# Kernel optimization log

Measured on AMD Instinct MI355X. Metric: run time of the kernel, lower is better.

## Reference

```python
import jax, jax.numpy as jnp
import numpy as np

B, S, E = 4, 2048, 1024
H = 16
D = E // H  # head_dim = 64


def setup_inputs() -> dict:
    key = jax.random.key(0)
    k1, k2, k3 = jax.random.split(key, 3)
    x = jax.random.normal(k1, (B, S, E), dtype=jnp.float32)
    w_qkv = jax.random.normal(k2, (E, 3 * E), dtype=jnp.float32) * (E ** -0.5)
    b_qkv = jnp.zeros((3 * E,), dtype=jnp.float32)
    w_proj = jax.random.normal(k3, (E, E), dtype=jnp.float32) * (E ** -0.5)
    b_proj = jnp.zeros((E,), dtype=jnp.float32)
    return {"x": x, "w_qkv": w_qkv, "b_qkv": b_qkv, "w_proj": w_proj, "b_proj": b_proj}


def reference(x, w_qkv, b_qkv, w_proj, b_proj):
    bsz, seq_len, emb = x.shape
    scale = D ** -0.5
    qkv = x @ w_qkv + b_qkv                      # [B,S,3E]
    q, k, v = jnp.split(qkv, 3, axis=2)
    # [B,S,E] -> [B,H,S,D]
    q = q.reshape(bsz, seq_len, H, D).transpose(0, 2, 1, 3)
    k = k.reshape(bsz, seq_len, H, D).transpose(0, 2, 1, 3)
    v = v.reshape(bsz, seq_len, H, D).transpose(0, 2, 1, 3)
    att = jnp.einsum('bhqd,bhkd->bhqk', q, k) * scale
    causal = jnp.tril(jnp.ones((seq_len, seq_len), dtype=bool))
    att = jnp.where(causal, att, -jnp.inf)
    att = jax.nn.softmax(att, axis=-1)
    y = jnp.einsum('bhqk,bhkd->bhqd', att, v)
    y = y.transpose(0, 2, 1, 3).reshape(bsz, seq_len, emb)
    return y @ w_proj + b_proj
```

## Files before the change

kernel.cpp:

```cpp
#include <hip/hip_runtime.h>
#include <hip/hip_bf16.h>
#include <stdint.h>

#define S_LEN 2048
#define EMB   1024
#define NH    16
#define HD    64

typedef unsigned short u16;
typedef __attribute__((ext_vector_type(4))) float f32x4;
typedef __attribute__((ext_vector_type(8))) short bf16x8;

typedef __attribute__((address_space(1))) const unsigned char gas_t;
typedef __attribute__((address_space(3))) unsigned char las_t;

static __device__ __forceinline__ void gld_lds16(const void* g, void* l) {
  __builtin_amdgcn_global_load_lds((gas_t*)g, (las_t*)l, 16, 0, 0);
}

static __device__ __forceinline__ u16 f2bf(float f) {
  unsigned int u = __builtin_bit_cast(unsigned int, f);
  u = u + 0x7fffu + ((u >> 16) & 1u);
  return (u16)(u >> 16);
}

static __device__ __forceinline__ float fexp2(float x) {
  float r;
  asm("v_exp_f32 %0, %1" : "=v"(r) : "v"(x));
  return r;
}

static __device__ __forceinline__ unsigned cvt_pk_bf16(float lo, float hi) {
  unsigned r;
  asm("v_cvt_pk_bf16_f32 %0, %1, %2" : "=v"(r) : "v"(lo), "v"(hi));
  return r;
}

static __device__ __forceinline__ float red4rows_max(float x) {
  unsigned u = __builtin_bit_cast(unsigned, x);
  auto r = __builtin_amdgcn_permlane32_swap(u, u, false, false);
  float y = fmaxf(__builtin_bit_cast(float, (unsigned)r[0]),
                  __builtin_bit_cast(float, (unsigned)r[1]));
  unsigned v = __builtin_bit_cast(unsigned, y);
  auto r2 = __builtin_amdgcn_permlane16_swap(v, v, false, false);
  return fmaxf(__builtin_bit_cast(float, (unsigned)r2[0]),
               __builtin_bit_cast(float, (unsigned)r2[1]));
}
static __device__ __forceinline__ float red4rows_sum(float x) {
  unsigned u = __builtin_bit_cast(unsigned, x);
  auto r = __builtin_amdgcn_permlane32_swap(u, u, false, false);
  float y = __builtin_bit_cast(float, (unsigned)r[0]) +
            __builtin_bit_cast(float, (unsigned)r[1]);
  unsigned v = __builtin_bit_cast(unsigned, y);
  auto r2 = __builtin_amdgcn_permlane16_swap(v, v, false, false);
  return __builtin_bit_cast(float, (unsigned)r2[0]) +
         __builtin_bit_cast(float, (unsigned)r2[1]);
}

__global__ __launch_bounds__(256) void k_cvt(const float* __restrict__ in,
                                             u16* __restrict__ out, int n4) {
  int i = blockIdx.x * blockDim.x + threadIdx.x;
  int stride = gridDim.x * blockDim.x;
  for (; i < n4; i += stride) {
    float4 f = ((const float4*)in)[i];
    ushort4 o;
    o.x = f2bf(f.x); o.y = f2bf(f.y); o.z = f2bf(f.z); o.w = f2bf(f.w);
    ((ushort4*)out)[i] = o;
  }
}

__global__ __launch_bounds__(256) void k_transpose_cvt(const float* __restrict__ W,
                                                       u16* __restrict__ WT,
                                                       int K, int N) {
  __shared__ u16 tile[64][68];
  const int c0 = blockIdx.x * 64, r0 = blockIdx.y * 64;
  const int t = threadIdx.x;
  const int tr = t >> 4, tc4 = (t & 15) * 4;
#pragma unroll
  for (int i = 0; i < 4; i++) {
    const int r = tr + 16 * i;
    float4 f = *(const float4*)&W[(size_t)(r0 + r) * N + c0 + tc4];
    ushort4 o;
    o.x = f2bf(f.x); o.y = f2bf(f.y); o.z = f2bf(f.z); o.w = f2bf(f.w);
    *(ushort4*)&tile[r][tc4] = o;
  }
  __syncthreads();
  const int oc = t >> 2, or0 = (t & 3) * 16;
  u16 vals[16];
#pragma unroll
  for (int j = 0; j < 16; j++) vals[j] = tile[or0 + j][oc];
  u16* dst = &WT[(size_t)(c0 + oc) * K + r0 + or0];
  *(uint4*)dst = *(const uint4*)&vals[0];
  *(uint4*)(dst + 8) = *(const uint4*)&vals[8];
}

template <int MODE>
__global__ __launch_bounds__(256) void k_gemm(const u16* __restrict__ A,
                                              const u16* __restrict__ BT,
                                              const float* __restrict__ bias,
                                              float* __restrict__ Cout,
                                              u16* __restrict__ q_ws,
                                              u16* __restrict__ k_ws,
                                              u16* __restrict__ v_t,
                                              int N, int K) {
  __shared__ u16 As[2][128 * 32];
  __shared__ u16 Bs[2][128 * 32];
  const int tid = threadIdx.x;
  const int w = tid >> 6, lane = tid & 63;
  const int wr = w >> 1, wc = w & 1;
  const int lrow = lane & 15, lk8 = (lane >> 4) * 8;
  const int brow = blockIdx.y * 128, bcol = blockIdx.x * 128;
  const int srow = lane >> 2;
  const int scol = (lane & 3) * 8;

  const f32x4 zero = {0.f, 0.f, 0.f, 0.f};
  f32x4 acc[4][4];
#pragma unroll
  for (int m = 0; m < 4; m++)
#pragma unroll
    for (int n = 0; n < 4; n++) acc[m][n] = zero;

  auto stage = [&](int kt, int buf) {
#pragma unroll
    for (int i = 0; i < 2; i++) {
      const int c = w * 2 + i;
      const int row = c * 16 + srow;
      gld_lds16(&A[(size_t)(brow + row) * K + kt + scol], (void*)(&As[buf][c * 512]));
      gld_lds16(&BT[(size_t)(bcol + row) * K + kt + scol], (void*)(&Bs[buf][c * 512]));
    }
  };

  const int NK = K >> 5;
  stage(0, 0);
  __syncthreads();
  for (int it = 0; it < NK; ++it) {
    const int cur = it & 1;
    if (it + 1 < NK) stage((it + 1) << 5, cur ^ 1);
    bf16x8 af[4], bfr[4];
#pragma unroll
    for (int mt = 0; mt < 4; mt++)
      af[mt] = *(const bf16x8*)&As[cur][(wr * 64 + mt * 16 + lrow) * 32 + lk8];
#pragma unroll
    for (int nt = 0; nt < 4; nt++)
      bfr[nt] = *(const bf16x8*)&Bs[cur][(wc * 64 + nt * 16 + lrow) * 32 + lk8];
    __builtin_amdgcn_s_setprio(1);
#pragma unroll
    for (int mt = 0; mt < 4; mt++)
#pragma unroll
      for (int nt = 0; nt < 4; nt++)
        acc[mt][nt] = __builtin_amdgcn_mfma_f32_16x16x32_bf16(af[mt], bfr[nt],
                                                              acc[mt][nt], 0, 0, 0);
    __builtin_amdgcn_s_setprio(0);
    __syncthreads();
  }

  if constexpr (MODE == 0) {
    const int which = bcol >> 10;
#pragma unroll
    for (int mt = 0; mt < 4; mt++)
#pragma unroll
      for (int nt = 0; nt < 4; nt++) {
        const int col = bcol + wc * 64 + nt * 16 + lrow;
        const int e = col & 1023;
        const int h = e >> 6, d = e & 63;
        const int row0 = brow + wr * 64 + mt * 16 + (lane >> 4) * 4;
        const int b = row0 >> 11, s0 = row0 & 2047;
        const size_t bh = (size_t)(b * NH + h);
        const float bv = bias[col];
        if (which == 2) {
          ushort4 pk;
          pk.x = f2bf(acc[mt][nt][0] + bv);
          pk.y = f2bf(acc[mt][nt][1] + bv);
          pk.z = f2bf(acc[mt][nt][2] + bv);
          pk.w = f2bf(acc[mt][nt][3] + bv);
          *(ushort4*)&v_t[(bh * HD + d) * S_LEN + s0] = pk;
        } else {
          u16* dst = which ? k_ws : q_ws;
#pragma unroll
          for (int r = 0; r < 4; r++)
            dst[(bh * S_LEN + s0 + r) * HD + d] = f2bf(acc[mt][nt][r] + bv);
        }
      }
  } else {
#pragma unroll
    for (int mt = 0; mt < 4; mt++)
#pragma unroll
      for (int nt = 0; nt < 4; nt++)
#pragma unroll
        for (int r = 0; r < 4; r++) {
          const int row = brow + wr * 64 + mt * 16 + (lane >> 4) * 4 + r;
          const int col = bcol + wc * 64 + nt * 16 + lrow;
          Cout[(size_t)row * N + col] = acc[mt][nt][r] + bias[col];
        }
  }
}

__global__ __launch_bounds__(256, 2) void k_attn(const u16* __restrict__ q_ws,
                                                 const u16* __restrict__ k_ws,
                                                 const u16* __restrict__ v_t,
                                                 u16* __restrict__ y) {
  __shared__ u16 Kl[2][64 * 64];
  __shared__ u16 Vl[2][64 * 64];
  const int tid = threadIdx.x;
  const int w = tid >> 6, lane = tid & 63;
  const int lrow = lane & 15, lk8 = (lane >> 4) * 8;
  const int g4 = (lane >> 4) * 4;
  const int pr = blockIdx.x;
  const int tileA = pr, tileB = 31 - pr;
  const int bh = blockIdx.y;
  const size_t base = (size_t)bh * S_LEN * HD;
  const float SC = 0.125f * 1.4426950408889634f;

  bf16x8 qfA[2], qfB[2];
#pragma unroll
  for (int ks = 0; ks < 2; ks++) {
    qfA[ks] = *(const bf16x8*)&q_ws[base + (size_t)(tileA * 64 + w * 16 + lrow) * HD + ks * 32 + lk8];
    qfB[ks] = *(const bf16x8*)&q_ws[base + (size_t)(tileB * 64 + w * 16 + lrow) * HD + ks * 32 + lk8];
  }

  const f32x4 zero = {0.f, 0.f, 0.f, 0.f};
  f32x4 oA[4], oB[4];
#pragma unroll
  for (int dt = 0; dt < 4; dt++) { oA[dt] = zero; oB[dt] = zero; }
  float mA = -1e30f, lA = 0.f, mB = -1e30f, lB = 0.f;

  auto stage = [&](int jb, int buf) {
#pragma unroll
    for (int i = 0; i < 2; i++) {
      const int c = w * 2 + i;
      const int row = c * 8 + (lane >> 3);
      const int blk = (lane & 7) ^ (row & 7);
      gld_lds16(&k_ws[base + (size_t)(jb * 64 + row) * HD + blk * 8],
                (void*)(&Kl[buf][c * 512]));
      gld_lds16(&v_t[base + (size_t)row * S_LEN + jb * 64 + blk * 8],
                (void*)(&Vl[buf][c * 512]));
    }
  };

  auto process = [&](const bf16x8 (&kf)[2][4], const bf16x8 (&vf)[2][4],
                     const bf16x8 (&qf)[2], f32x4 (&o)[4], float& m_run,
                     float& l_run, bool maskDiag) {
    f32x4 sa[4];
#pragma unroll
    for (int nt = 0; nt < 4; nt++) sa[nt] = zero;
    __builtin_amdgcn_s_setprio(1);
#pragma unroll
    for (int ks = 0; ks < 2; ks++)
#pragma unroll
      for (int nt = 0; nt < 4; nt++)
        sa[nt] = __builtin_amdgcn_mfma_f32_16x16x32_bf16(kf[ks][nt], qf[ks], sa[nt], 0, 0, 0);
    __builtin_amdgcn_s_setprio(0);

    float sv[4][4];
    if (maskDiag) {
#pragma unroll
      for (int nt = 0; nt < 4; nt++)
#pragma unroll
        for (int r = 0; r < 4; r++) {
          float x = sa[nt][r] * SC;
          if ((nt * 16 + g4 + r) > (w * 16 + lrow)) x = -3.0e38f;
          sv[nt][r] = x;
        }
    } else {
#pragma unroll
      for (int nt = 0; nt < 4; nt++)
#pragma unroll
        for (int r = 0; r < 4; r++) sv[nt][r] = sa[nt][r] * SC;
    }

    float mx = fmaxf(fmaxf(fmaxf(sv[0][0], sv[0][1]), fmaxf(sv[0][2], sv[0][3])),
                     fmaxf(fmaxf(sv[1][0], sv[1][1]), fmaxf(sv[1][2], sv[1][3])));
    mx = fmaxf(mx,
               fmaxf(fmaxf(fmaxf(sv[2][0], sv[2][1]), fmaxf(sv[2][2], sv[2][3])),
                     fmaxf(fmaxf(sv[3][0], sv[3][1]), fmaxf(sv[3][2], sv[3][3]))));
    mx = red4rows_max(mx);
    const bool nogrow = __all(mx <= m_run + 8.0f);
    float mn = m_run;
    if (!nogrow) {
      mn = fmaxf(m_run, mx);
      const float alpha = fexp2(m_run - mn);
      l_run *= alpha;
#pragma unroll
      for (int dt = 0; dt < 4; dt++) o[dt] *= alpha;
      m_run = mn;
    }
    float sum = 0.f;
#pragma unroll
    for (int nt = 0; nt < 4; nt++)
#pragma unroll
      for (int r = 0; r < 4; r++) {
        const float p = fexp2(sv[nt][r] - mn);
        sv[nt][r] = p;
        sum += p;
      }
    sum = red4rows_sum(sum);
    l_run += sum;

    unsigned pk[4][2];
#pragma unroll
    for (int nt = 0; nt < 4; nt++) {
      pk[nt][0] = cvt_pk_bf16(sv[nt][0], sv[nt][1]);
      pk[nt][1] = cvt_pk_bf16(sv[nt][2], sv[nt][3]);
    }
    union { unsigned u[4]; bf16x8 v; } c0, c1;
    {
      auto r0 = __builtin_amdgcn_permlane32_swap(pk[0][0], pk[1][0], false, false);
      auto s0 = __builtin_amdgcn_permlane16_swap(r0[0], r0[1], false, false);
      auto r1 = __builtin_amdgcn_permlane32_swap(pk[0][1], pk[1][1], false, false);
      auto s1 = __builtin_amdgcn_permlane16_swap(r1[0], r1[1], false, false);
      c0.u[0] = s0[0]; c0.u[1] = s1[0]; c0.u[2] = s0[1]; c0.u[3] = s1[1];
      auto r2 = __builtin_amdgcn_permlane32_swap(pk[2][0], pk[3][0], false, false);
      auto s2 = __builtin_amdgcn_permlane16_swap(r2[0], r2[1], false, false);
      auto r3 = __builtin_amdgcn_permlane32_swap(pk[2][1], pk[3][1], false, false);
      auto s3 = __builtin_amdgcn_permlane16_swap(r3[0], r3[1], false, false);
      c1.u[0] = s2[0]; c1.u[1] = s3[0]; c1.u[2] = s2[1]; c1.u[3] = s3[1];
    }
    bf16x8 pfrag[2] = {c0.v, c1.v};

    __builtin_amdgcn_s_setprio(1);
#pragma unroll
    for (int ks = 0; ks < 2; ks++)
#pragma unroll
      for (int dt = 0; dt < 4; dt++)
        o[dt] = __builtin_amdgcn_mfma_f32_16x16x32_bf16(vf[ks][dt], pfrag[ks], o[dt], 0, 0, 0);
    __builtin_amdgcn_s_setprio(0);
  };

  stage(0, 0);
  __syncthreads();
  for (int jb = 0; jb <= tileB; jb++) {
    const int cur = jb & 1;
    if (jb < tileB) stage(jb + 1, cur ^ 1);
    bf16x8 kf[2][4], vf[2][4];
#pragma unroll
    for (int ks = 0; ks < 2; ks++)
#pragma unroll
      for (int nt = 0; nt < 4; nt++) {
        const int kvr = nt * 16 + lrow;
        const int blk = (ks * 4 + (lane >> 4)) ^ (kvr & 7);
        kf[ks][nt] = *(const bf16x8*)&Kl[cur][kvr * 64 + blk * 8];
        vf[ks][nt] = *(const bf16x8*)&Vl[cur][kvr * 64 + blk * 8];
      }
    process(kf, vf, qfB, oB, mB, lB, jb == tileB);
    if (jb <= tileA) process(kf, vf, qfA, oA, mA, lA, jb == tileA);
    __syncthreads();
  }

  const int b = bh >> 4, h = bh & 15;
  const float invA = 1.0f / lA;
  const float invB = 1.0f / lB;
  const int qgA = tileA * 64 + w * 16 + lrow;
  const int qgB = tileB * 64 + w * 16 + lrow;
#pragma unroll
  for (int dt = 0; dt < 4; dt++) {
    ushort4 sA, sB;
    sA.x = f2bf(oA[dt][0] * invA); sA.y = f2bf(oA[dt][1] * invA);
    sA.z = f2bf(oA[dt][2] * invA); sA.w = f2bf(oA[dt][3] * invA);
    sB.x = f2bf(oB[dt][0] * invB); sB.y = f2bf(oB[dt][1] * invB);
    sB.z = f2bf(oB[dt][2] * invB); sB.w = f2bf(oB[dt][3] * invB);
    *(ushort4*)&y[(size_t)(b * S_LEN + qgA) * EMB + h * HD + dt * 16 + g4] = sA;
    *(ushort4*)&y[(size_t)(b * S_LEN + qgB) * EMB + h * HD + dt * 16 + g4] = sB;
  }
}

extern "C" void kernel_launch(void* const* d_in, const int* in_sizes, int n_in,
                              void* d_out, int out_size, void* d_ws, size_t ws_size,
                              hipStream_t stream) {
  const float* x      = (const float*)d_in[0];
  const float* w_qkv  = (const float*)d_in[1];
  const float* b_qkv  = (const float*)d_in[2];
  const float* w_proj = (const float*)d_in[3];
  const float* b_proj = (const float*)d_in[4];
  float* out = (float*)d_out;

  char* ws = (char*)d_ws;
  u16* wqkvT  = (u16*)(ws);
  u16* wprojT = (u16*)(ws + 6291456);
  u16* xb     = (u16*)(ws + 8388608);
  u16* q_ws   = (u16*)(ws + 25165824);
  u16* k_ws   = (u16*)(ws + 41943040);
  u16* v_t    = (u16*)(ws + 58720256);
  u16* y_att  = xb;

  k_cvt<<<dim3(1024), dim3(256), 0, stream>>>(x, xb, (8192 * 1024) / 4);
  k_transpose_cvt<<<dim3(48, 16), dim3(256), 0, stream>>>(w_qkv, wqkvT, 1024, 3072);
  k_transpose_cvt<<<dim3(16, 16), dim3(256), 0, stream>>>(w_proj, wprojT, 1024, 1024);
  k_gemm<0><<<dim3(24, 64), dim3(256), 0, stream>>>(xb, wqkvT, b_qkv, nullptr,
                                                    q_ws, k_ws, v_t, 3072, 1024);
  k_attn<<<dim3(16, 64), dim3(256), 0, stream>>>(q_ws, k_ws, v_t, y_att);
  k_gemm<1><<<dim3(8, 64), dim3(256), 0, stream>>>(y_att, wprojT, b_proj, out,
                                                   nullptr, nullptr, nullptr, 1024, 1024);
}
```

Before: 197.5 us.

## Merge prep kernels into one launch and fold softmax scale into exp FMA

```diff
diff --git a/kernel.cpp b/kernel.cpp
--- a/kernel.cpp
+++ b/kernel.cpp
@@ -8,6 +8,7 @@
 #define HD    64
 
 typedef unsigned short u16;
+typedef __attribute__((ext_vector_type(2))) float f32x2;
 typedef __attribute__((ext_vector_type(4))) float f32x4;
 typedef __attribute__((ext_vector_type(8))) short bf16x8;
 
@@ -33,6 +34,12 @@
 static __device__ __forceinline__ unsigned cvt_pk_bf16(float lo, float hi) {
   unsigned r;
   asm("v_cvt_pk_bf16_f32 %0, %1, %2" : "=v"(r) : "v"(lo), "v"(hi));
+  return r;
+}
+
+static __device__ __forceinline__ f32x2 pk_add(f32x2 a, f32x2 b) {
+  f32x2 r;
+  asm("v_pk_add_f32 %0, %1, %2" : "=v"(r) : "v"(a), "v"(b));
   return r;
 }
 
@@ -57,24 +64,38 @@
          __builtin_bit_cast(float, (unsigned)r2[1]);
 }
 
-__global__ __launch_bounds__(256) void k_cvt(const float* __restrict__ in,
-                                             u16* __restrict__ out, int n4) {
-  int i = blockIdx.x * blockDim.x + threadIdx.x;
-  int stride = gridDim.x * blockDim.x;
-  for (; i < n4; i += stride) {
-    float4 f = ((const float4*)in)[i];
-    ushort4 o;
-    o.x = f2bf(f.x); o.y = f2bf(f.y); o.z = f2bf(f.z); o.w = f2bf(f.w);
-    ((ushort4*)out)[i] = o;
-  }
-}
-
-__global__ __launch_bounds__(256) void k_transpose_cvt(const float* __restrict__ W,
-                                                       u16* __restrict__ WT,
-                                                       int K, int N) {
+__global__ __launch_bounds__(256) void k_prep(const float* __restrict__ x,
+                                              u16* __restrict__ xb,
+                                              const float* __restrict__ w_qkv,
+                                              u16* __restrict__ wqkvT,
+                                              const float* __restrict__ w_proj,
+                                              u16* __restrict__ wprojT) {
   __shared__ u16 tile[64][68];
-  const int c0 = blockIdx.x * 64, r0 = blockIdx.y * 64;
+  const int bid = blockIdx.x;
   const int t = threadIdx.x;
+  if (bid < 1024) {
+    const int n4 = (8192 * 1024) / 4;
+    int i = bid * 256 + t;
+    for (; i < n4; i += 1024 * 256) {
+      float4 f = ((const float4*)x)[i];
+      ushort4 o;
+      o.x = f2bf(f.x); o.y = f2bf(f.y); o.z = f2bf(f.z); o.w = f2bf(f.w);
+      ((ushort4*)xb)[i] = o;
+    }
+    return;
+  }
+  const float* W;
+  u16* WT;
+  int c0, r0, K, N;
+  if (bid < 1792) {
+    const int idx = bid - 1024;
+    W = w_qkv; WT = wqkvT; K = 1024; N = 3072;
+    c0 = (idx % 48) * 64; r0 = (idx / 48) * 64;
+  } else {
+    const int idx = bid - 1792;
+    W = w_proj; WT = wprojT; K = 1024; N = 1024;
+    c0 = (idx & 15) * 64; r0 = (idx >> 4) * 64;
+  }
   const int tr = t >> 4, tc4 = (t & 15) * 4;
 #pragma unroll
   for (int i = 0; i < 4; i++) {
@@ -256,16 +277,13 @@
 #pragma unroll
       for (int nt = 0; nt < 4; nt++)
 #pragma unroll
-        for (int r = 0; r < 4; r++) {
-          float x = sa[nt][r] * SC;
-          if ((nt * 16 + g4 + r) > (w * 16 + lrow)) x = -3.0e38f;
-          sv[nt][r] = x;
-        }
+        for (int r = 0; r < 4; r++)
+          sv[nt][r] = ((nt * 16 + g4 + r) > (w * 16 + lrow)) ? -3.0e38f : sa[nt][r];
     } else {
 #pragma unroll
       for (int nt = 0; nt < 4; nt++)
 #pragma unroll
-        for (int r = 0; r < 4; r++) sv[nt][r] = sa[nt][r] * SC;
+        for (int r = 0; r < 4; r++) sv[nt][r] = sa[nt][r];
     }
 
     float mx = fmaxf(fmaxf(fmaxf(sv[0][0], sv[0][1]), fmaxf(sv[0][2], sv[0][3])),
@@ -274,46 +292,57 @@
                fmaxf(fmaxf(fmaxf(sv[2][0], sv[2][1]), fmaxf(sv[2][2], sv[2][3])),
                      fmaxf(fmaxf(sv[3][0], sv[3][1]), fmaxf(sv[3][2], sv[3][3]))));
     mx = red4rows_max(mx);
-    const bool nogrow = __all(mx <= m_run + 8.0f);
+    const float mxs = mx * SC;
+    const bool nogrow = __all(mxs <= m_run + 8.0f);
     float mn = m_run;
     if (!nogrow) {
-      mn = fmaxf(m_run, mx);
+      mn = fmaxf(m_run, mxs);
       const float alpha = fexp2(m_run - mn);
       l_run *= alpha;
 #pragma unroll
       for (int dt = 0; dt < 4; dt++) o[dt] *= alpha;
       m_run = mn;
     }
-    float sum = 0.f;
+    const float nmn = -mn;
+    f32x2 p2[4][2];
 #pragma unroll
     for (int nt = 0; nt < 4; nt++)
 #pragma unroll
-      for (int r = 0; r < 4; r++) {
-        const float p = fexp2(sv[nt][r] - mn);
-        sv[nt][r] = p;
-        sum += p;
+      for (int h = 0; h < 2; h++) {
+        const float a = fexp2(__builtin_fmaf(sv[nt][2 * h], SC, nmn));
+        const float b = fexp2(__builtin_fmaf(sv[nt][2 * h + 1], SC, nmn));
+        f32x2 p; p[0] = a; p[1] = b;
+        p2[nt][h] = p;
       }
+    f32x2 s0 = pk_add(p2[0][0], p2[0][1]);
+    f32x2 s1 = pk_add(p2[1][0], p2[1][1]);
+    f32x2 s2 = pk_add(p2[2][0], p2[2][1]);
+    f32x2 s3 = pk_add(p2[3][0], p2[3][1]);
+    s0 = pk_add(s0, s1);
+    s2 = pk_add(s2, s3);
+    s0 = pk_add(s0, s2);
+    float sum = s0[0] + s0[1];
     sum = red4rows_sum(sum);
     l_run += sum;
 
     unsigned pk[4][2];
 #pragma unroll
     for (int nt = 0; nt < 4; nt++) {
-      pk[nt][0] = cvt_pk_bf16(sv[nt][0], sv[nt][1]);
-      pk[nt][1] = cvt_pk_bf16(sv[nt][2], sv[nt][3]);
+      pk[nt][0] = cvt_pk_bf16(p2[nt][0][0], p2[nt][0][1]);
+      pk[nt][1] = cvt_pk_bf16(p2[nt][1][0], p2[nt][1][1]);
     }
     union { unsigned u[4]; bf16x8 v; } c0, c1;
     {
       auto r0 = __builtin_amdgcn_permlane32_swap(pk[0][0], pk[1][0], false, false);
-      auto s0 = __builtin_amdgcn_permlane16_swap(r0[0], r0[1], false, false);
+      auto s0p = __builtin_amdgcn_permlane16_swap(r0[0], r0[1], false, false);
       auto r1 = __builtin_amdgcn_permlane32_swap(pk[0][1], pk[1][1], false, false);
-      auto s1 = __builtin_amdgcn_permlane16_swap(r1[0], r1[1], false, false);
-      c0.u[0] = s0[0]; c0.u[1] = s1[0]; c0.u[2] = s0[1]; c0.u[3] = s1[1];
+      auto s1p = __builtin_amdgcn_permlane16_swap(r1[0], r1[1], false, false);
+      c0.u[0] = s0p[0]; c0.u[1] = s1p[0]; c0.u[2] = s0p[1]; c0.u[3] = s1p[1];
       auto r2 = __builtin_amdgcn_permlane32_swap(pk[2][0], pk[3][0], false, false);
-      auto s2 = __builtin_amdgcn_permlane16_swap(r2[0], r2[1], false, false);
+      auto s2p = __builtin_amdgcn_permlane16_swap(r2[0], r2[1], false, false);
       auto r3 = __builtin_amdgcn_permlane32_swap(pk[2][1], pk[3][1], false, false);
-      auto s3 = __builtin_amdgcn_permlane16_swap(r3[0], r3[1], false, false);
-      c1.u[0] = s2[0]; c1.u[1] = s3[0]; c1.u[2] = s2[1]; c1.u[3] = s3[1];
+      auto s3p = __builtin_amdgcn_permlane16_swap(r3[0], r3[1], false, false);
+      c1.u[0] = s2p[0]; c1.u[1] = s3p[0]; c1.u[2] = s2p[1]; c1.u[3] = s3p[1];
     }
     bf16x8 pfrag[2] = {c0.v, c1.v};
 
@@ -353,13 +382,13 @@
   const int qgB = tileB * 64 + w * 16 + lrow;
 #pragma unroll
   for (int dt = 0; dt < 4; dt++) {
-    ushort4 sA, sB;
-    sA.x = f2bf(oA[dt][0] * invA); sA.y = f2bf(oA[dt][1] * invA);
-    sA.z = f2bf(oA[dt][2] * invA); sA.w = f2bf(oA[dt][3] * invA);
-    sB.x = f2bf(oB[dt][0] * invB); sB.y = f2bf(oB[dt][1] * invB);
-    sB.z = f2bf(oB[dt][2] * invB); sB.w = f2bf(oB[dt][3] * invB);
-    *(ushort4*)&y[(size_t)(b * S_LEN + qgA) * EMB + h * HD + dt * 16 + g4] = sA;
-    *(ushort4*)&y[(size_t)(b * S_LEN + qgB) * EMB + h * HD + dt * 16 + g4] = sB;
+    uint2 pa, pb;
+    pa.x = cvt_pk_bf16(oA[dt][0] * invA, oA[dt][1] * invA);
+    pa.y = cvt_pk_bf16(oA[dt][2] * invA, oA[dt][3] * invA);
+    pb.x = cvt_pk_bf16(oB[dt][0] * invB, oB[dt][1] * invB);
+    pb.y = cvt_pk_bf16(oB[dt][2] * invB, oB[dt][3] * invB);
+    *(uint2*)&y[(size_t)(b * S_LEN + qgA) * EMB + h * HD + dt * 16 + g4] = pa;
+    *(uint2*)&y[(size_t)(b * S_LEN + qgB) * EMB + h * HD + dt * 16 + g4] = pb;
   }
 }
 
@@ -382,9 +411,7 @@
   u16* v_t    = (u16*)(ws + 58720256);
   u16* y_att  = xb;
 
-  k_cvt<<<dim3(1024), dim3(256), 0, stream>>>(x, xb, (8192 * 1024) / 4);
-  k_transpose_cvt<<<dim3(48, 16), dim3(256), 0, stream>>>(w_qkv, wqkvT, 1024, 3072);
-  k_transpose_cvt<<<dim3(16, 16), dim3(256), 0, stream>>>(w_proj, wprojT, 1024, 1024);
+  k_prep<<<dim3(2048), dim3(256), 0, stream>>>(x, xb, w_qkv, wqkvT, w_proj, wprojT);
   k_gemm<0><<<dim3(24, 64), dim3(256), 0, stream>>>(xb, wqkvT, b_qkv, nullptr,
                                                     q_ws, k_ws, v_t, 3072, 1024);
   k_attn<<<dim3(16, 64), dim3(256), 0, stream>>>(q_ws, k_ws, v_t, y_att);
```

New measurement: 193.6 us. -2.0%, faster.
